# Optimization experiments

Hardware: AMD Instinct MI355X
Metric: run time of the kernel (lower is better)

Reference implementation:

```python
import jax, jax.numpy as jnp
import numpy as np

B = 4096
M = 4            # n_modalities
T = 8            # n_tasks
D = 1024         # feature_dim per modality
DIN = D * M      # concat feature dim = 4096
H = 256          # hidden_dim
H2 = 2 * H       # 512
TEMP = 1.0
EPS = 1e-5


def _layernorm(x, g, b):
    # LayerNorm over last axis (torch nn.LayerNorm semantics, eps=1e-5)
    mu = jnp.mean(x, axis=-1, keepdims=True)
    var = jnp.mean(jnp.square(x - mu), axis=-1, keepdims=True)
    return (x - mu) * jax.lax.rsqrt(var + EPS) * g + b


def setup_inputs() -> dict:
    key = jax.random.key(0)
    ks = jax.random.split(key, 16)
    s = 0.02
    return {
        "f0": jax.random.normal(ks[0], (B, D), jnp.float32),
        "f1": jax.random.normal(ks[1], (B, D), jnp.float32),
        "f2": jax.random.normal(ks[2], (B, D), jnp.float32),
        "f3": jax.random.normal(ks[3], (B, D), jnp.float32),
        # per-task feature-net params (stacked ModuleList)
        "W1": jax.random.normal(ks[4], (T, DIN, H2), jnp.float32) * s,
        "b1": jnp.zeros((T, H2), jnp.float32),
        "g1": jnp.ones((T, H2), jnp.float32),
        "be1": jnp.zeros((T, H2), jnp.float32),
        "W2": jax.random.normal(ks[5], (T, H2, H), jnp.float32) * s,
        "b2": jnp.zeros((T, H), jnp.float32),
        "g2": jnp.ones((T, H), jnp.float32),
        "be2": jnp.zeros((T, H), jnp.float32),
        "task_emb": jax.random.normal(ks[6], (T, H), jnp.float32),
        # per-task weight-net params (Linear(2H -> M))
        "Ww": jax.random.normal(ks[7], (T, H2, M), jnp.float32) * s,
        "bw": jnp.zeros((T, M), jnp.float32),
        "task_ids": jax.random.randint(ks[8], (B,), 0, T, jnp.int32),
    }


def reference(f0, f1, f2, f3, W1, b1, g1, be1, W2, b2, g2, be2, task_emb, Ww, bw, task_ids):
    x = jnp.concatenate([f0, f1, f2, f3], axis=1)              # [B, DIN]
    # compute all-task feature nets densely (T is small), then gather per sample
    h = jnp.einsum('bd,tdh->bth', x, W1) + b1[None]            # [B, T, 2H]
    h = jax.nn.relu(_layernorm(h, g1[None], be1[None]))
    h = jnp.einsum('bth,thk->btk', h, W2) + b2[None]           # [B, T, H]
    h = jax.nn.relu(_layernorm(h, g2[None], be2[None]))
    hid = jnp.take_along_axis(h, task_ids[:, None, None], axis=1)[:, 0]  # [B, H]
    te = task_emb[task_ids]                                    # [B, H]
    comb = jnp.concatenate([hid, te], axis=1)                  # [B, 2H]
    # per-sample gather of small weight-net matrices (irregular access)
    raw = jnp.einsum('bh,bhm->bm', comb, Ww[task_ids]) + bw[task_ids]    # [B, M]
    return jax.nn.softmax(raw / TEMP, axis=1)
```

## Files before the change

### kernel.cpp

```cpp
#include <hip/hip_runtime.h>
#include <stdint.h>

#define B_N 4096
#define T_N 8
#define DIN 4096
#define H2C 512
#define HC 256
#define NWG1 1024
#define NWG2 264
#define SPLITK1 4

typedef __attribute__((ext_vector_type(8))) short bf16x8;
typedef __attribute__((ext_vector_type(4))) float f32x4;

static __device__ __forceinline__ unsigned short f2bf(float f) {
    union { float f; uint32_t u; } v; v.f = f;
    uint32_t u = v.u;
    uint32_t r = (u + 0x7FFFu + ((u >> 16) & 1u)) >> 16;
    return (unsigned short)r;
}

static __device__ __forceinline__ float bf2f(uint32_t h) {
    union { uint32_t u; float f; } v; v.u = h << 16; return v.f;
}

static __device__ __forceinline__ uint32_t pk2(float a, float b) {
    uint32_t r;
    asm volatile("v_cvt_pk_bf16_f32 %0, %1, %2" : "=v"(r) : "v"(a), "v"(b));
    return r;
}

static __device__ __forceinline__ void gl2lds16(const unsigned short* g, unsigned short* l) {
    __builtin_amdgcn_global_load_lds(
        (const __attribute__((address_space(1))) unsigned int*)(g),
        (__attribute__((address_space(3))) unsigned int*)(l), 16, 0, 0);
}

static __device__ __forceinline__ void gl2lds16f(const float* g, float* l) {
    __builtin_amdgcn_global_load_lds(
        (const __attribute__((address_space(1))) unsigned int*)(g),
        (__attribute__((address_space(3))) unsigned int*)(l), 16, 0, 0);
}

static __device__ __forceinline__ int xcd_remap(int bid, int nwg) {
    int xcd = bid & 7, idx = bid >> 3;
    int q = nwg >> 3, r = nwg & 7;
    return (xcd < r ? xcd * (q + 1) : r * (q + 1) + (xcd - r) * q) + idx;
}

__launch_bounds__(256)
__global__ void k_pre(const float* __restrict__ W1, const float* __restrict__ W2,
                      const int* __restrict__ task_ids,
                      const float* __restrict__ temb, const float* __restrict__ Ww,
                      const float* __restrict__ bw,
                      unsigned short* __restrict__ W1t, unsigned short* __restrict__ W2t,
                      int* __restrict__ order, int* __restrict__ tiles, int* __restrict__ bmap,
                      int* __restrict__ tiles2, int* __restrict__ ntile2,
                      float* __restrict__ tb) {
    int blk = blockIdx.x, tid = threadIdx.x;
    if (blk == 0) {
        __shared__ unsigned long long wtot[4][2];
        __shared__ int lc[T_N], lseg[T_N], tb1p[T_N + 1], tb2p[T_N + 1];
        int lane = tid & 63, wv = tid >> 6;
        int4 a0 = *(const int4*)(task_ids + tid * 16);
        int4 a1 = *(const int4*)(task_ids + tid * 16 + 4);
        int4 a2 = *(const int4*)(task_ids + tid * 16 + 8);
        int4 a3 = *(const int4*)(task_ids + tid * 16 + 12);
        int myt[16] = {a0.x, a0.y, a0.z, a0.w, a1.x, a1.y, a1.z, a1.w,
                       a2.x, a2.y, a2.z, a2.w, a3.x, a3.y, a3.z, a3.w};
        unsigned long long ph0 = 0, ph1 = 0;
        #pragma unroll
        for (int i = 0; i < 16; ++i) {
            int t = myt[i];
            if (t < 4) ph0 += 1ull << (t * 16); else ph1 += 1ull << ((t - 4) * 16);
        }
        unsigned long long s0 = ph0, s1 = ph1;
        for (int o = 1; o < 64; o <<= 1) {
            unsigned long long u0 = __shfl_up(s0, o);
            unsigned long long u1 = __shfl_up(s1, o);
            if (lane >= o) { s0 += u0; s1 += u1; }
        }
        if (lane == 63) { wtot[wv][0] = s0; wtot[wv][1] = s1; }
        __syncthreads();
        unsigned long long e0 = s0 - ph0, e1 = s1 - ph1;
        for (int w2 = 0; w2 < wv; ++w2) { e0 += wtot[w2][0]; e1 += wtot[w2][1]; }
        if (tid == 0) {
            unsigned long long t0 = 0, t1 = 0;
            for (int w2 = 0; w2 < 4; ++w2) { t0 += wtot[w2][0]; t1 += wtot[w2][1]; }
            int s = 0;
            for (int t = 0; t < T_N; ++t) {
                int c = (int)((t < 4 ? (t0 >> (t * 16)) : (t1 >> ((t - 4) * 16))) & 0xFFFF);
                lc[t] = c; lseg[t] = s; s += c;
            }
            int q1 = 0, q2 = 0;
            for (int t = 0; t < T_N; ++t) {
                tb1p[t] = q1; tb2p[t] = q2;
                q1 += (lc[t] + 127) >> 7; q2 += (lc[t] + 15) >> 4;
            }
            tb1p[T_N] = q1; tb2p[T_N] = q2;
            ntile2[0] = q2;
        }
        __syncthreads();
        unsigned long long r0 = e0, r1 = e1;
        #pragma unroll
        for (int i = 0; i < 16; ++i) {
            int t = myt[i], rk;
            if (t < 4) { rk = (int)((r0 >> (t * 16)) & 0xFFFF); r0 += 1ull << (t * 16); }
            else { int u = t - 4; rk = (int)((r1 >> (u * 16)) & 0xFFFF); r1 += 1ull << (u * 16); }
            order[lseg[t] + rk] = tid * 16 + i;
        }
        int n1 = tb1p[T_N], n2 = tb2p[T_N];
        for (int e = tid; e < n1; e += 256) {
            int t = 0; while (e >= tb1p[t + 1]) ++t;
            int rr = (e - tb1p[t]) << 7;
            tiles[3 * e] = t; tiles[3 * e + 1] = lseg[t] + rr;
            int rem = lc[t] - rr; tiles[3 * e + 2] = rem < 128 ? rem : 128;
        }
        for (int e = tid; e < n2; e += 256) {
            int t = 0; while (e >= tb2p[t + 1]) ++t;
            int rr = (e - tb2p[t]) << 4;
            tiles2[3 * e] = t; tiles2[3 * e + 1] = lseg[t] + rr;
            int rem = lc[t] - rr; tiles2[3 * e + 2] = rem < 16 ? rem : 16;
        }
        for (int s = tid; s < NWG1; s += 256) {
            int t = s & 7, j = s >> 3;
            int base = tb1p[t], nt = tb1p[t + 1] - base;
            bmap[s] = (j < nt * 16) ? (((base + (j >> 4)) << 4) | (j & 15)) : -1;
        }
        __syncthreads();
        if (tid == 0) {
            int freeslot = 0;
            for (int t = 0; t < T_N; ++t) {
                int base = tb1p[t], nt = tb1p[t + 1] - base;
                for (int j = 128; j < nt * 16; ++j) {
                    while (bmap[freeslot] >= 0) ++freeslot;
                    bmap[freeslot] = ((base + (j >> 4)) << 4) | (j & 15);
                }
            }
        }
        for (int t = wv; t < T_N; t += 4) {
            int m = lane & 3, hb = (lane >> 2) * 16;
            float s = 0.f;
            for (int h = 0; h < 16; ++h)
                s += temb[t * HC + hb + h] * Ww[((size_t)t * H2C + HC + hb + h) * 4 + m];
            for (int o = 4; o < 64; o <<= 1) s += __shfl_xor(s, o);
            if (lane < 4) tb[t * 4 + lane] = s + bw[t * 4 + lane];
        }
        return;
    }
    __shared__ float tile[64][65];
    const float* ip; unsigned short* op; int R, C, bx, by, t;
    if (blk < 4097) {
        int idx = blk - 1; bx = idx & 63; by = (idx >> 6) & 7; t = idx >> 9;
        R = DIN; C = H2C;
        ip = W1 + (size_t)t * R * C; op = W1t + (size_t)t * R * C;
    } else {
        int idx = blk - 4097; bx = idx & 7; by = (idx >> 3) & 3; t = idx >> 5;
        R = H2C; C = HC;
        ip = W2 + (size_t)t * R * C; op = W2t + (size_t)t * R * C;
    }
    int r0 = bx * 64, c0 = by * 64;
    int lr = tid >> 4, lc4 = (tid & 15) * 4;
    #pragma unroll
    for (int i = 0; i < 4; ++i) {
        float4 v = *(const float4*)&ip[(size_t)(r0 + lr + i * 16) * C + c0 + lc4];
        tile[lr + i * 16][lc4 + 0] = v.x;
        tile[lr + i * 16][lc4 + 1] = v.y;
        tile[lr + i * 16][lc4 + 2] = v.z;
        tile[lr + i * 16][lc4 + 3] = v.w;
    }
    __syncthreads();
    int r4 = (tid & 15) * 4;
    #pragma unroll
    for (int i = 0; i < 4; ++i) {
        int cc = i * 16 + (tid >> 4);
        uint2 wv;
        wv.x = (uint32_t)f2bf(tile[r4 + 0][cc]) | ((uint32_t)f2bf(tile[r4 + 1][cc]) << 16);
        wv.y = (uint32_t)f2bf(tile[r4 + 2][cc]) | ((uint32_t)f2bf(tile[r4 + 3][cc]) << 16);
        *(uint2*)&op[(size_t)(c0 + cc) * R + r0 + r4] = wv;
    }
}

__launch_bounds__(256)
__global__ void k_gemm1(const float* __restrict__ f0, const float* __restrict__ f1,
                        const float* __restrict__ f2, const float* __restrict__ f3,
                        const unsigned short* __restrict__ Bt,
                        unsigned short* __restrict__ Cb16, const int* __restrict__ order,
                        const int* __restrict__ tiles, const int* __restrict__ bmap) {
    int e = bmap[blockIdx.x];
    if (e < 0) return;
    int tix = e >> 4, sub = e & 15;
    int ct = sub >> 2, kc = sub & 3;
    int t = tiles[3 * tix], prow = tiles[3 * tix + 1], rows = tiles[3 * tix + 2];
    int kb = kc * (DIN / SPLITK1);
    const float* fsrc = (kc == 0) ? f0 : (kc == 1) ? f1 : (kc == 2) ? f2 : f3;

    __shared__ float ldsA[2][128 * 32];
    __shared__ unsigned short ldsB[2][128 * 32];

    int tid = threadIdx.x, lane = tid & 63, w = tid >> 6;
    int wm = w >> 1, wn = w & 1;

    const float* pA4[4];
    #pragma unroll
    for (int j = 0; j < 4; ++j) {
        int slot = j * 256 + tid;
        int row = slot >> 3, gd = slot & 7;
        int rl = row < rows ? row : rows - 1;
        pA4[j] = fsrc + (size_t)order[prow + rl] * 1024 + (gd ^ (row & 7)) * 4;
    }
    const unsigned short* pB[2];
    #pragma unroll
    for (int j = 0; j < 2; ++j) {
        int slot = j * 256 + tid;
        int row = slot >> 2, gd = slot & 3;
        pB[j] = Bt + ((size_t)t * H2C + ct * 128 + row) * DIN + kb + (gd ^ ((row >> 1) & 3)) * 8;
    }

    auto stage = [&](int buf, int it) {
        float* dA = &ldsA[buf][(size_t)w * 256];
        unsigned short* dB = &ldsB[buf][(size_t)w * 512];
        #pragma unroll
        for (int j = 0; j < 4; ++j) gl2lds16f(pA4[j] + it * 32, dA + j * 1024);
        #pragma unroll
        for (int j = 0; j < 2; ++j) gl2lds16(pB[j] + it * 32, dB + j * 2048);
    };

    f32x4 acc[4][4];
    #pragma unroll
    for (int m = 0; m < 4; ++m)
        #pragma unroll
        for (int n = 0; n < 4; ++n)
            acc[m][n] = (f32x4){0.f, 0.f, 0.f, 0.f};

    constexpr int NIT = (DIN / SPLITK1) / 32;
    stage(0, 0);
    __syncthreads();
    int cur = 0;
    int g = lane >> 4, lrow = lane & 15;
    for (int it = 0; it < NIT; ++it) {
        if (it + 1 < NIT) stage(cur ^ 1, it + 1);
        const float* Af = &ldsA[cur][0];
        const unsigned short* Bs = &ldsB[cur][0];
        bf16x8 af[4], bfv[4];
        #pragma unroll
        for (int m = 0; m < 4; ++m) {
            int row = wm * 64 + m * 16 + lrow;
            float4 lo = *(const float4*)(Af + row * 32 + (((2 * g) ^ (row & 7)) * 4));
            float4 hi = *(const float4*)(Af + row * 32 + (((2 * g + 1) ^ (row & 7)) * 4));
            union { uint4 u; bf16x8 b; } cv;
            cv.u.x = pk2(lo.x, lo.y); cv.u.y = pk2(lo.z, lo.w);
            cv.u.z = pk2(hi.x, hi.y); cv.u.w = pk2(hi.z, hi.w);
            af[m] = cv.b;
        }
        #pragma unroll
        for (int n = 0; n < 4; ++n) {
            int row = wn * 64 + n * 16 + lrow;
            bfv[n] = *(const bf16x8*)&Bs[row * 32 + ((g ^ ((row >> 1) & 3)) * 8)];
        }
        #pragma unroll
        for (int m = 0; m < 4; ++m)
            #pragma unroll
            for (int n = 0; n < 4; ++n)
                acc[m][n] = __builtin_amdgcn_mfma_f32_16x16x32_bf16(af[m], bfv[n], acc[m][n], 0, 0, 0);
        __syncthreads();
        cur ^= 1;
    }

    unsigned short* Cb = Cb16 + (size_t)kc * B_N * H2C;
    #pragma unroll
    for (int m = 0; m < 4; ++m) {
        #pragma unroll
        for (int n = 0; n < 4; ++n) {
            int col = ct * 128 + wn * 64 + n * 16 + (lane & 15);
            #pragma unroll
            for (int j = 0; j < 4; ++j) {
                int row = wm * 64 + m * 16 + (lane >> 4) * 4 + j;
                if (row < rows)
                    Cb[(size_t)(prow + row) * H2C + col] = f2bf(acc[m][n][j]);
            }
        }
    }
}

__launch_bounds__(256)
__global__ void k_gemm2f(const unsigned short* __restrict__ h1p, const unsigned short* __restrict__ W2t,
                         const float* __restrict__ b1, const float* __restrict__ g1,
                         const float* __restrict__ be1,
                         const float* __restrict__ b2, const float* __restrict__ g2,
                         const float* __restrict__ be2,
                         const float* __restrict__ Ww, const float* __restrict__ tb,
                         const int* __restrict__ order,
                         const int* __restrict__ tiles2, const int* __restrict__ ntile2,
                         float* __restrict__ out) {
    __shared__ unsigned short Asm[16 * 512];
    __shared__ unsigned short Bsm[2][256 * 32];
    __shared__ float red[16][4][4];

    int id = xcd_remap(blockIdx.x, NWG2);
    if (id >= ntile2[0]) return;
    int t = tiles2[3 * id], prow = tiles2[3 * id + 1], rows = tiles2[3 * id + 2];
    int tid = threadIdx.x, lane = tid & 63, w = tid >> 6;

    {
        int r = tid >> 4;
        int rl = r < rows ? r : rows - 1;
        int c0 = (tid & 15) * 32;
        const unsigned short* p0 = h1p + (size_t)(prow + rl) * H2C + c0;
        const float* pb = b1 + t * H2C + c0;
        float x[32];
        float s = 0.f, sq = 0.f;
        #pragma unroll
        for (int i = 0; i < 32; i += 8) {
            uint4 u0 = *(const uint4*)(p0 + i);
            uint4 u1 = *(const uint4*)(p0 + (size_t)B_N * H2C + i);
            uint4 u2 = *(const uint4*)(p0 + (size_t)2 * B_N * H2C + i);
            uint4 u3 = *(const uint4*)(p0 + (size_t)3 * B_N * H2C + i);
            uint32_t w0[4] = {u0.x, u0.y, u0.z, u0.w};
            uint32_t w1[4] = {u1.x, u1.y, u1.z, u1.w};
            uint32_t w2[4] = {u2.x, u2.y, u2.z, u2.w};
            uint32_t w3[4] = {u3.x, u3.y, u3.z, u3.w};
            float4 c0v = *(const float4*)(pb + i);
            float4 c1v = *(const float4*)(pb + i + 4);
            float cv[8] = {c0v.x, c0v.y, c0v.z, c0v.w, c1v.x, c1v.y, c1v.z, c1v.w};
            #pragma unroll
            for (int q = 0; q < 4; ++q) {
                float v0 = bf2f(w0[q] & 0xFFFFu) + bf2f(w1[q] & 0xFFFFu)
                         + bf2f(w2[q] & 0xFFFFu) + bf2f(w3[q] & 0xFFFFu) + cv[2 * q];
                float v1 = bf2f(w0[q] >> 16) + bf2f(w1[q] >> 16)
                         + bf2f(w2[q] >> 16) + bf2f(w3[q] >> 16) + cv[2 * q + 1];
                x[i + 2 * q] = v0; x[i + 2 * q + 1] = v1;
                s += v0 + v1; sq += v0 * v0 + v1 * v1;
            }
        }
        #pragma unroll
        for (int o = 1; o < 16; o <<= 1) { s += __shfl_xor(s, o); sq += __shfl_xor(sq, o); }
        float mean = s * (1.f / H2C);
        float var = sq * (1.f / H2C) - mean * mean;
        float rstd = rsqrtf(var + 1e-5f);
        const float* pg = g1 + t * H2C + c0;
        const float* pe = be1 + t * H2C + c0;
        #pragma unroll
        for (int i = 0; i < 32; i += 8) {
            unsigned short y[8];
            #pragma unroll
            for (int q = 0; q < 8; q += 4) {
                float4 gv = *(const float4*)(pg + i + q);
                float4 ev = *(const float4*)(pe + i + q);
                y[q + 0] = f2bf(fmaxf((x[i + q + 0] - mean) * rstd * gv.x + ev.x, 0.f));
                y[q + 1] = f2bf(fmaxf((x[i + q + 1] - mean) * rstd * gv.y + ev.y, 0.f));
                y[q + 2] = f2bf(fmaxf((x[i + q + 2] - mean) * rstd * gv.z + ev.z, 0.f));
                y[q + 3] = f2bf(fmaxf((x[i + q + 3] - mean) * rstd * gv.w + ev.w, 0.f));
            }
            uint4 wv;
            wv.x = (uint32_t)y[0] | ((uint32_t)y[1] << 16);
            wv.y = (uint32_t)y[2] | ((uint32_t)y[3] << 16);
            wv.z = (uint32_t)y[4] | ((uint32_t)y[5] << 16);
            wv.w = (uint32_t)y[6] | ((uint32_t)y[7] << 16);
            int g = (c0 + i) >> 3;
            *(uint4*)&Asm[r * 512 + ((g ^ (r & 7)) * 8)] = wv;
        }
    }

    auto stageB = [&](int buf, int it) {
        #pragma unroll
        for (int j = 0; j < 4; ++j) {
            int G = j * 256 + tid;
            int row = G >> 2, g = G & 3;
            int colg = g ^ (row & 3);
            gl2lds16(W2t + ((size_t)t * HC + row) * H2C + it * 32 + colg * 8,
                     &Bsm[buf][(j * 256 + w * 64) * 8]);
        }
    };

    stageB(0, 0);
    __syncthreads();

    f32x4 acc[4];
    #pragma unroll
    for (int n = 0; n < 4; ++n) acc[n] = (f32x4){0.f, 0.f, 0.f, 0.f};

    for (int it = 0; it < 16; ++it) {
        if (it + 1 < 16) stageB((it + 1) & 1, it + 1);
        const unsigned short* Bs = &Bsm[it & 1][0];
        int g = lane >> 4;
        int arow = lane & 15;
        bf16x8 af = *(const bf16x8*)&Asm[arow * 512 + (((it * 4 + g) ^ (arow & 7)) * 8)];
        #pragma unroll
        for (int n = 0; n < 4; ++n) {
            int brow = w * 64 + n * 16 + arow;
            bf16x8 bv = *(const bf16x8*)&Bs[brow * 32 + ((g ^ (brow & 3)) * 8)];
            acc[n] = __builtin_amdgcn_mfma_f32_16x16x32_bf16(af, bv, acc[n], 0, 0, 0);
        }
        __syncthreads();
    }

    float b2v[4], g2v[4], e2v[4];
    float4 wv[4];
    #pragma unroll
    for (int n = 0; n < 4; ++n) {
        int col = w * 64 + n * 16 + (lane & 15);
        b2v[n] = b2[t * HC + col];
        g2v[n] = g2[t * HC + col];
        e2v[n] = be2[t * HC + col];
        wv[n] = *(const float4*)&Ww[((size_t)t * H2C + col) * 4];
    }
    float s4[4], q4[4];
    #pragma unroll
    for (int j = 0; j < 4; ++j) {
        float s = 0.f, sq = 0.f;
        #pragma unroll
        for (int n = 0; n < 4; ++n) {
            float xv = acc[n][j] + b2v[n];
            s += xv; sq += xv * xv;
        }
        #pragma unroll
        for (int o = 1; o < 16; o <<= 1) { s += __shfl_xor(s, o); sq += __shfl_xor(sq, o); }
        s4[j] = s; q4[j] = sq;
    }
    if ((lane & 15) == 0) {
        #pragma unroll
        for (int j = 0; j < 4; ++j) {
            int r = (lane >> 4) * 4 + j;
            red[r][w][0] = s4[j];
            red[r][w][1] = q4[j];
        }
    }
    __syncthreads();
    float mean[4], rstd[4];
    #pragma unroll
    for (int j = 0; j < 4; ++j) {
        int r = (lane >> 4) * 4 + j;
        float S = red[r][0][0] + red[r][1][0] + red[r][2][0] + red[r][3][0];
        float SQ = red[r][0][1] + red[r][1][1] + red[r][2][1] + red[r][3][1];
        mean[j] = S * (1.f / HC);
        float var = SQ * (1.f / HC) - mean[j] * mean[j];
        rstd[j] = rsqrtf(var + 1e-5f);
    }
    float p[4][4];
    #pragma unroll
    for (int j = 0; j < 4; ++j) {
        p[j][0] = 0.f; p[j][1] = 0.f; p[j][2] = 0.f; p[j][3] = 0.f;
        #pragma unroll
        for (int n = 0; n < 4; ++n) {
            float yv = fmaxf((acc[n][j] + b2v[n] - mean[j]) * rstd[j] * g2v[n] + e2v[n], 0.f);
            p[j][0] += yv * wv[n].x; p[j][1] += yv * wv[n].y;
            p[j][2] += yv * wv[n].z; p[j][3] += yv * wv[n].w;
        }
        #pragma unroll
        for (int m = 0; m < 4; ++m)
            #pragma unroll
            for (int o = 1; o < 16; o <<= 1) p[j][m] += __shfl_xor(p[j][m], o);
    }
    __syncthreads();
    if ((lane & 15) == 0) {
        #pragma unroll
        for (int j = 0; j < 4; ++j) {
            int r = (lane >> 4) * 4 + j;
            red[r][w][0] = p[j][0]; red[r][w][1] = p[j][1];
            red[r][w][2] = p[j][2]; red[r][w][3] = p[j][3];
        }
    }
    __syncthreads();
    if (tid < 16 && tid < rows) {
        float raw[4];
        #pragma unroll
        for (int m = 0; m < 4; ++m)
            raw[m] = red[tid][0][m] + red[tid][1][m] + red[tid][2][m] + red[tid][3][m] + tb[t * 4 + m];
        float mx = fmaxf(fmaxf(raw[0], raw[1]), fmaxf(raw[2], raw[3]));
        float e0 = expf(raw[0] - mx), e1 = expf(raw[1] - mx);
        float e2 = expf(raw[2] - mx), e3 = expf(raw[3] - mx);
        float si = 1.f / (e0 + e1 + e2 + e3);
        *(float4*)(out + (size_t)order[prow + tid] * 4) = make_float4(e0 * si, e1 * si, e2 * si, e3 * si);
    }
}

extern "C" void kernel_launch(void* const* d_in, const int* in_sizes, int n_in,
                              void* d_out, int out_size, void* d_ws, size_t ws_size,
                              hipStream_t stream) {
    const float* f0 = (const float*)d_in[0];
    const float* f1 = (const float*)d_in[1];
    const float* f2 = (const float*)d_in[2];
    const float* f3 = (const float*)d_in[3];
    const float* W1 = (const float*)d_in[4];
    const float* b1 = (const float*)d_in[5];
    const float* g1 = (const float*)d_in[6];
    const float* be1 = (const float*)d_in[7];
    const float* W2 = (const float*)d_in[8];
    const float* b2 = (const float*)d_in[9];
    const float* g2 = (const float*)d_in[10];
    const float* be2 = (const float*)d_in[11];
    const float* temb = (const float*)d_in[12];
    const float* Ww = (const float*)d_in[13];
    const float* bw = (const float*)d_in[14];
    const int* task_ids = (const int*)d_in[15];
    float* out = (float*)d_out;

    char* ws = (char*)d_ws;
    size_t off = 0;
    auto walloc = [&](size_t bytes) -> void* {
        void* p = ws + off;
        off = (off + bytes + 255) & ~(size_t)255;
        return p;
    };
    float* tb = (float*)walloc(128);
    int* tiles = (int*)walloc(64 * 3 * 4);
    int* bmap = (int*)walloc(NWG1 * 4);
    int* tiles2 = (int*)walloc(272 * 3 * 4);
    int* ntile2 = (int*)walloc(4);
    int* order = (int*)walloc((size_t)B_N * 4);
    unsigned short* W1t = (unsigned short*)walloc((size_t)T_N * H2C * DIN * 2);
    unsigned short* W2t = (unsigned short*)walloc((size_t)T_N * HC * H2C * 2);
    unsigned short* h1p = (unsigned short*)walloc((size_t)SPLITK1 * B_N * H2C * 2);

    k_pre<<<4353, 256, 0, stream>>>(W1, W2, task_ids, temb, Ww, bw,
                                    W1t, W2t, order, tiles, bmap, tiles2, ntile2, tb);
    k_gemm1<<<NWG1, 256, 0, stream>>>(f0, f1, f2, f3, W1t, h1p, order, tiles, bmap);
    k_gemm2f<<<NWG2, 256, 0, stream>>>(h1p, W2t, b1, g1, be1, b2, g2, be2, Ww, tb,
                                       order, tiles2, ntile2, out);
}
```

Before: 85.04 us.

## Load GEMM1 operands directly from global memory, dropping LDS staging

The first GEMM kernel no longer stages A and B tiles through double-buffered LDS with global_load_lds and barriers. Each lane now reads its MFMA fragments straight from global memory (relying on L1/L2 caching for reuse across waves), with a partial unroll of the K loop. The launch bounds also request three blocks per CU. This removes LDS traffic and synchronisation, at the cost of redundant global loads across waves and less latency hiding, since there is no explicit prefetch.

Result: slower. 154.5 us (+81.7%).

```diff
diff --git a/kernel.cpp b/kernel.cpp
--- a/kernel.cpp
+++ b/kernel.cpp
@@ -31,12 +31,6 @@
 }
 
 static __device__ __forceinline__ void gl2lds16(const unsigned short* g, unsigned short* l) {
-    __builtin_amdgcn_global_load_lds(
-        (const __attribute__((address_space(1))) unsigned int*)(g),
-        (__attribute__((address_space(3))) unsigned int*)(l), 16, 0, 0);
-}
-
-static __device__ __forceinline__ void gl2lds16f(const float* g, float* l) {
     __builtin_amdgcn_global_load_lds(
         (const __attribute__((address_space(1))) unsigned int*)(g),
         (__attribute__((address_space(3))) unsigned int*)(l), 16, 0, 0);
@@ -181,7 +175,7 @@
     }
 }
 
-__launch_bounds__(256)
+__launch_bounds__(256, 3)
 __global__ void k_gemm1(const float* __restrict__ f0, const float* __restrict__ f1,
                         const float* __restrict__ f2, const float* __restrict__ f3,
                         const unsigned short* __restrict__ Bt,
@@ -195,36 +189,24 @@
     int kb = kc * (DIN / SPLITK1);
     const float* fsrc = (kc == 0) ? f0 : (kc == 1) ? f1 : (kc == 2) ? f2 : f3;
 
-    __shared__ float ldsA[2][128 * 32];
-    __shared__ unsigned short ldsB[2][128 * 32];
-
     int tid = threadIdx.x, lane = tid & 63, w = tid >> 6;
     int wm = w >> 1, wn = w & 1;
-
-    const float* pA4[4];
-    #pragma unroll
-    for (int j = 0; j < 4; ++j) {
-        int slot = j * 256 + tid;
-        int row = slot >> 3, gd = slot & 7;
+    int lrow = lane & 15;
+    int lk = (lane >> 4) * 8;
+
+    const float* pA[4];
+    #pragma unroll
+    for (int m = 0; m < 4; ++m) {
+        int row = wm * 64 + m * 16 + lrow;
         int rl = row < rows ? row : rows - 1;
-        pA4[j] = fsrc + (size_t)order[prow + rl] * 1024 + (gd ^ (row & 7)) * 4;
-    }
-    const unsigned short* pB[2];
-    #pragma unroll
-    for (int j = 0; j < 2; ++j) {
-        int slot = j * 256 + tid;
-        int row = slot >> 2, gd = slot & 3;
-        pB[j] = Bt + ((size_t)t * H2C + ct * 128 + row) * DIN + kb + (gd ^ ((row >> 1) & 3)) * 8;
-    }
-
-    auto stage = [&](int buf, int it) {
-        float* dA = &ldsA[buf][(size_t)w * 256];
-        unsigned short* dB = &ldsB[buf][(size_t)w * 512];
-        #pragma unroll
-        for (int j = 0; j < 4; ++j) gl2lds16f(pA4[j] + it * 32, dA + j * 1024);
-        #pragma unroll
-        for (int j = 0; j < 2; ++j) gl2lds16(pB[j] + it * 32, dB + j * 2048);
-    };
+        pA[m] = fsrc + (size_t)order[prow + rl] * 1024 + lk;
+    }
+    const unsigned short* pBf[4];
+    #pragma unroll
+    for (int n = 0; n < 4; ++n) {
+        int col = ct * 128 + wn * 64 + n * 16 + lrow;
+        pBf[n] = Bt + ((size_t)t * H2C + col) * DIN + kb + lk;
+    }
 
     f32x4 acc[4][4];
     #pragma unroll
@@ -233,38 +215,27 @@
         for (int n = 0; n < 4; ++n)
             acc[m][n] = (f32x4){0.f, 0.f, 0.f, 0.f};
 
-    constexpr int NIT = (DIN / SPLITK1) / 32;
-    stage(0, 0);
-    __syncthreads();
-    int cur = 0;
-    int g = lane >> 4, lrow = lane & 15;
-    for (int it = 0; it < NIT; ++it) {
-        if (it + 1 < NIT) stage(cur ^ 1, it + 1);
-        const float* Af = &ldsA[cur][0];
-        const unsigned short* Bs = &ldsB[cur][0];
+    #pragma unroll 2
+    for (int it = 0; it < 32; ++it) {
+        int ko = it * 32;
         bf16x8 af[4], bfv[4];
         #pragma unroll
         for (int m = 0; m < 4; ++m) {
-            int row = wm * 64 + m * 16 + lrow;
-            float4 lo = *(const float4*)(Af + row * 32 + (((2 * g) ^ (row & 7)) * 4));
-            float4 hi = *(const float4*)(Af + row * 32 + (((2 * g + 1) ^ (row & 7)) * 4));
+            float4 lo = *(const float4*)(pA[m] + ko);
+            float4 hi = *(const float4*)(pA[m] + ko + 4);
             union { uint4 u; bf16x8 b; } cv;
             cv.u.x = pk2(lo.x, lo.y); cv.u.y = pk2(lo.z, lo.w);
             cv.u.z = pk2(hi.x, hi.y); cv.u.w = pk2(hi.z, hi.w);
             af[m] = cv.b;
         }
         #pragma unroll
-        for (int n = 0; n < 4; ++n) {
-            int row = wn * 64 + n * 16 + lrow;
-            bfv[n] = *(const bf16x8*)&Bs[row * 32 + ((g ^ ((row >> 1) & 3)) * 8)];
-        }
+        for (int n = 0; n < 4; ++n)
+            bfv[n] = *(const bf16x8*)(pBf[n] + ko);
         #pragma unroll
         for (int m = 0; m < 4; ++m)
             #pragma unroll
             for (int n = 0; n < 4; ++n)
                 acc[m][n] = __builtin_amdgcn_mfma_f32_16x16x32_bf16(af[m], bfv[n], acc[m][n], 0, 0, 0);
-        __syncthreads();
-        cur ^= 1;
     }
 
     unsigned short* Cb = Cb16 + (size_t)kc * B_N * H2C;
```
